# Kernel optimization log

Measured on AMD Instinct MI355X. Metric: run time of the kernel, lower is better.

Reference implementation:

```python
import jax, jax.numpy as jnp
import numpy as np

HIDDEN = 512
HEADS = 8
NORM = 1.0 / np.sqrt(HIDDEN // HEADS)  # torch: 1/sqrt(tensor(dim_k)//head) = 1/8


def setup_inputs() -> dict:
    key = jax.random.key(0)
    ks = jax.random.split(key, 14)
    B, N, D = 2, 2048, HIDDEN
    s = 0.02
    d = {
        "x_re": jax.random.normal(ks[0], (B, N, D), dtype=jnp.float32),
        "x_im": jax.random.normal(ks[1], (B, N, D), dtype=jnp.float32),
    }
    names = ["Wq_re", "Wq_im", "bq_re", "bq_im",
             "Wk_re", "Wk_im", "bk_re", "bk_im",
             "Wv_re", "Wv_im", "bv_re", "bv_im"]
    for i, nm in enumerate(names):
        shape = (D, D) if nm.startswith("W") else (D,)
        d[nm] = jax.random.normal(ks[2 + i], shape, dtype=jnp.float32) * s
    return d


def reference(x_re, x_im,
              Wq_re, Wq_im, bq_re, bq_im,
              Wk_re, Wk_im, bk_re, bk_im,
              Wv_re, Wv_im, bv_re, bv_im):
    B, N, D = x_re.shape
    h, dk = HEADS, D // HEADS
    x = jax.lax.complex(x_re, x_im)
    Wq = jax.lax.complex(Wq_re, Wq_im); bq = jax.lax.complex(bq_re, bq_im)
    Wk = jax.lax.complex(Wk_re, Wk_im); bk = jax.lax.complex(bk_re, bk_im)
    Wv = jax.lax.complex(Wv_re, Wv_im); bv = jax.lax.complex(bv_re, bv_im)

    def proj(W, b):  # torch nn.Linear: x @ W.T + b, then split heads -> [B,h,N,dk]
        y = x @ W.T + b
        return y.reshape(B, N, h, dk).transpose(0, 2, 1, 3)

    q, k, v = proj(Wq, bq), proj(Wk, bk), proj(Wv, bv)
    # complex matmul (no conjugation, matching torch.matmul), scaled
    dist = jnp.einsum("bhnd,bhmd->bhnm", q, k) * NORM
    probs = jax.nn.softmax(jnp.abs(dist), axis=-1).astype(jnp.complex64)
    att = jnp.einsum("bhnm,bhmd->bhnd", probs, v)
    att = att.transpose(0, 2, 1, 3).reshape(B, N, D)
    # real-view output [B, N, D, 2]
    return jnp.stack([att.real, att.imag], axis=-1)
```

## Files before the change

### kernel.cpp

```cpp
#include <hip/hip_runtime.h>
#include <hip/hip_bf16.h>
#include <math.h>

#define B_ 2
#define N_ 2048
#define D_ 512
#define H_ 8
#define DK_ 64
#define M_ (B_ * N_)

typedef short s16x8 __attribute__((ext_vector_type(8)));
typedef short s16x4 __attribute__((ext_vector_type(4)));
typedef float fx4   __attribute__((ext_vector_type(4)));
typedef int   ix4   __attribute__((ext_vector_type(4)));

static __device__ __forceinline__ short f2bf(float f) {
    __hip_bfloat16 h = __float2bfloat16(f);
    return __builtin_bit_cast(short, h);
}
static __device__ __forceinline__ float bf2f(short s) {
    unsigned int u = ((unsigned int)(unsigned short)s) << 16;
    return __builtin_bit_cast(float, u);
}
static __device__ __forceinline__ float fexp2(float x) {
#if __has_builtin(__builtin_amdgcn_exp2f)
    return __builtin_amdgcn_exp2f(x);
#else
    return exp2f(x);
#endif
}
static __device__ __forceinline__ float fsqrt_(float x) {
#if __has_builtin(__builtin_amdgcn_sqrtf)
    return __builtin_amdgcn_sqrtf(x);
#else
    return sqrtf(x);
#endif
}
static __device__ __forceinline__ int pack_tr(float a, float b) {
    unsigned ua = __builtin_bit_cast(unsigned, a);
    unsigned ub = __builtin_bit_cast(unsigned, b);
    return (int)((ua >> 16) | (ub & 0xFFFF0000u));
}

#define MFMA16(a, b, c) __builtin_amdgcn_mfma_f32_16x16x32_bf16(a, b, c, 0, 0, 0)

#define C2_ 0.18033688f
#define M0_ 16.0f

__global__ __launch_bounds__(256, 2)
void qkproj_mfma(const float* __restrict__ xr, const float* __restrict__ xi,
                 const float* __restrict__ W0r, const float* __restrict__ W0i,
                 const float* __restrict__ b0r, const float* __restrict__ b0i,
                 const float* __restrict__ W1r, const float* __restrict__ W1i,
                 const float* __restrict__ b1r, const float* __restrict__ b1i,
                 short* __restrict__ o0r, short* __restrict__ o0i,
                 short* __restrict__ o1r, short* __restrict__ o1i)
{
    __shared__ short sA[2][128][40];
    __shared__ short sB[2][64][40];

    const int tid = threadIdx.x;
    const int w = tid >> 6, l = tid & 63, lg = l >> 4, lc = l & 15;
    const int wr = w >> 1, wc = w & 1;
    const int bn = blockIdx.x, bm = blockIdx.y, z = blockIdx.z;
    const float* Wr = z ? W1r : W0r;
    const float* Wi = z ? W1i : W0i;
    const float* br = z ? b1r : b0r;
    const float* bi = z ? b1i : b0i;
    short* outr = z ? o1r : o0r;
    short* outi = z ? o1i : o0i;

    const int srow = tid >> 3, scol = (tid & 7) * 4;
    int aoff = (bm * 128 + srow) * D_ + scol;
    int boff = (bn * 64 + srow) * D_ + scol;

    float4 rA[8], rB[4];
    auto issue = [&]() {
#pragma unroll
        for (int u = 0; u < 8; ++u) {
            const float* src = (u >= 4) ? xi : xr;
            rA[u] = *(const float4*)&src[aoff + (u & 3) * 32 * D_];
        }
#pragma unroll
        for (int u = 0; u < 4; ++u) {
            const float* src = (u >= 2) ? Wi : Wr;
            rB[u] = *(const float4*)&src[boff + (u & 1) * 32 * D_];
        }
        aoff += 32; boff += 32;
    };

    fx4 Cre[4][2], Cim[4][2];
#pragma unroll
    for (int mf = 0; mf < 4; ++mf)
#pragma unroll
        for (int nf = 0; nf < 2; ++nf)
#pragma unroll
            for (int j = 0; j < 4; ++j) { Cre[mf][nf][j] = 0.f; Cim[mf][nf][j] = 0.f; }

    issue();
    for (int k0 = 0; k0 < D_; k0 += 32) {
        __syncthreads();
#pragma unroll
        for (int u = 0; u < 8; ++u) {
            int comp = u >> 2, row = (u & 3) * 32 + srow;
            float vv[4] = {rA[u].x, rA[u].y, rA[u].z, rA[u].w};
            s16x4 hv;
#pragma unroll
            for (int q = 0; q < 4; ++q) hv[q] = f2bf(vv[q]);
            *(s16x4*)&sA[comp][row][scol] = hv;
        }
#pragma unroll
        for (int u = 0; u < 4; ++u) {
            int comp = u >> 1, row = (u & 1) * 32 + srow;
            float vv[4] = {rB[u].x, rB[u].y, rB[u].z, rB[u].w};
            s16x4 hv;
#pragma unroll
            for (int q = 0; q < 4; ++q) hv[q] = f2bf(vv[q]);
            *(s16x4*)&sB[comp][row][scol] = hv;
        }
        __syncthreads();
        if (k0 + 32 < D_) issue();

        s16x8 a[2][4];
#pragma unroll
        for (int comp = 0; comp < 2; ++comp)
#pragma unroll
            for (int mf = 0; mf < 4; ++mf)
                a[comp][mf] = *(const s16x8*)&sA[comp][wr * 64 + mf * 16 + lc][lg * 8];
        s16x8 bfr[2][2], bin[2];
#pragma unroll
        for (int comp = 0; comp < 2; ++comp)
#pragma unroll
            for (int nf = 0; nf < 2; ++nf)
                bfr[comp][nf] = *(const s16x8*)&sB[comp][wc * 32 + nf * 16 + lc][lg * 8];
#pragma unroll
        for (int nf = 0; nf < 2; ++nf) bin[nf] = bfr[1][nf] ^ (short)0x8000;

        __builtin_amdgcn_s_setprio(1);
#pragma unroll
        for (int mf = 0; mf < 4; ++mf)
#pragma unroll
            for (int nf = 0; nf < 2; ++nf) {
                Cre[mf][nf] = MFMA16(a[0][mf], bfr[0][nf], Cre[mf][nf]);
                Cre[mf][nf] = MFMA16(a[1][mf], bin[nf],    Cre[mf][nf]);
                Cim[mf][nf] = MFMA16(a[0][mf], bfr[1][nf], Cim[mf][nf]);
                Cim[mf][nf] = MFMA16(a[1][mf], bfr[0][nf], Cim[mf][nf]);
            }
        __builtin_amdgcn_s_setprio(0);
    }

    const int bb = (bm * 128) >> 11;
#pragma unroll
    for (int nf = 0; nf < 2; ++nf) {
        const int c = bn * 64 + wc * 32 + nf * 16 + lc;
        const float brv = br[c], biv = bi[c];
        const int h = c >> 6, dd = c & 63;
        const int n00 = (bm * 128 + wr * 64 + lg * 4) & (N_ - 1);
        size_t obase = (((size_t)(bb * H_ + h) * N_) + n00) * DK_ + dd;
#pragma unroll
        for (int mf = 0; mf < 4; ++mf)
#pragma unroll
            for (int j = 0; j < 4; ++j) {
                size_t o = obase + (size_t)(mf * 16 + j) * DK_;
                outr[o] = f2bf(Cre[mf][nf][j] + brv);
                outi[o] = f2bf(Cim[mf][nf][j] + biv);
            }
    }
}

__global__ __launch_bounds__(256, 2)
void vproj_mfma(const float* __restrict__ xr, const float* __restrict__ xi,
                const float* __restrict__ Wr, const float* __restrict__ Wi,
                const float* __restrict__ br, const float* __restrict__ bi,
                short* __restrict__ outr, short* __restrict__ outi)
{
    __shared__ short sA[2][2][64][40];
    __shared__ short sB[2][2][64][40];

    const int tid = threadIdx.x;
    const int w = tid >> 6, l = tid & 63, lg = l >> 4, lc = l & 15;
    const int wr = w >> 1, wc = w & 1;
    const int bn = blockIdx.x, bm = blockIdx.y;

    const int srow = tid >> 3, scol = (tid & 7) * 4;
    int aoff = (bm * 64 + srow) * D_ + scol;
    int boff = (bn * 64 + srow) * D_ + scol;

    float4 rA[4], rB[4];
    auto issue = [&]() {
#pragma unroll
        for (int u = 0; u < 4; ++u) {
            const float* src = (u >= 2) ? xi : xr;
            rA[u] = *(const float4*)&src[aoff + (u & 1) * 32 * D_];
        }
#pragma unroll
        for (int u = 0; u < 4; ++u) {
            const float* src = (u >= 2) ? Wi : Wr;
            rB[u] = *(const float4*)&src[boff + (u & 1) * 32 * D_];
        }
        aoff += 32; boff += 32;
    };

    fx4 Cre[2][2], Cim[2][2];
#pragma unroll
    for (int mf = 0; mf < 2; ++mf)
#pragma unroll
        for (int nf = 0; nf < 2; ++nf)
#pragma unroll
            for (int j = 0; j < 4; ++j) { Cre[mf][nf][j] = 0.f; Cim[mf][nf][j] = 0.f; }

    issue();
    for (int k0 = 0; k0 < D_; k0 += 32) {
        __syncthreads();
#pragma unroll
        for (int u = 0; u < 4; ++u) {
            int comp = u >> 1, row = (u & 1) * 32 + srow;
            float vv[4] = {rA[u].x, rA[u].y, rA[u].z, rA[u].w};
            s16x4 hv, lv;
#pragma unroll
            for (int q = 0; q < 4; ++q) {
                short hh = f2bf(vv[q]);
                hv[q] = hh;
                lv[q] = f2bf(vv[q] - bf2f(hh));
            }
            *(s16x4*)&sA[comp][0][row][scol] = hv;
            *(s16x4*)&sA[comp][1][row][scol] = lv;
        }
#pragma unroll
        for (int u = 0; u < 4; ++u) {
            int comp = u >> 1, row = (u & 1) * 32 + srow;
            float vv[4] = {rB[u].x, rB[u].y, rB[u].z, rB[u].w};
            s16x4 hv, lv;
#pragma unroll
            for (int q = 0; q < 4; ++q) {
                short hh = f2bf(vv[q]);
                hv[q] = hh;
                lv[q] = f2bf(vv[q] - bf2f(hh));
            }
            *(s16x4*)&sB[comp][0][row][scol] = hv;
            *(s16x4*)&sB[comp][1][row][scol] = lv;
        }
        __syncthreads();
        if (k0 + 32 < D_) issue();

        s16x8 a[2][2][2];
#pragma unroll
        for (int comp = 0; comp < 2; ++comp)
#pragma unroll
            for (int s = 0; s < 2; ++s)
#pragma unroll
                for (int mf = 0; mf < 2; ++mf)
                    a[comp][s][mf] = *(const s16x8*)&sA[comp][s][wr * 32 + mf * 16 + lc][lg * 8];
        s16x8 bfr[2][2][2], bin[2][2];
#pragma unroll
        for (int comp = 0; comp < 2; ++comp)
#pragma unroll
            for (int s = 0; s < 2; ++s)
#pragma unroll
                for (int nf = 0; nf < 2; ++nf)
                    bfr[comp][s][nf] = *(const s16x8*)&sB[comp][s][wc * 32 + nf * 16 + lc][lg * 8];
#pragma unroll
        for (int s = 0; s < 2; ++s)
#pragma unroll
            for (int nf = 0; nf < 2; ++nf)
                bin[s][nf] = bfr[1][s][nf] ^ (short)0x8000;

        __builtin_amdgcn_s_setprio(1);
#pragma unroll
        for (int mf = 0; mf < 2; ++mf)
#pragma unroll
            for (int nf = 0; nf < 2; ++nf) {
                fx4 cr = Cre[mf][nf], ci = Cim[mf][nf];
                cr = MFMA16(a[0][0][mf], bfr[0][0][nf], cr);
                cr = MFMA16(a[1][0][mf], bin[0][nf],    cr);
                ci = MFMA16(a[0][0][mf], bfr[1][0][nf], ci);
                ci = MFMA16(a[1][0][mf], bfr[0][0][nf], ci);
                cr = MFMA16(a[0][0][mf], bfr[0][1][nf], cr);
                cr = MFMA16(a[0][1][mf], bfr[0][0][nf], cr);
                cr = MFMA16(a[1][0][mf], bin[1][nf],    cr);
                cr = MFMA16(a[1][1][mf], bin[0][nf],    cr);
                ci = MFMA16(a[0][0][mf], bfr[1][1][nf], ci);
                ci = MFMA16(a[0][1][mf], bfr[1][0][nf], ci);
                ci = MFMA16(a[1][0][mf], bfr[0][1][nf], ci);
                ci = MFMA16(a[1][1][mf], bfr[0][0][nf], ci);
                Cre[mf][nf] = cr; Cim[mf][nf] = ci;
            }
        __builtin_amdgcn_s_setprio(0);
    }

    const int bb = (bm * 64) >> 11;
#pragma unroll
    for (int nf = 0; nf < 2; ++nf) {
        const int c = bn * 64 + wc * 32 + nf * 16 + lc;
        const float brv = br[c], biv = bi[c];
        const int h = c >> 6, dd = c & 63;
#pragma unroll
        for (int mf = 0; mf < 2; ++mf) {
            int m0 = bm * 64 + wr * 32 + mf * 16 + lg * 4;
            int n0 = m0 & (N_ - 1);
            s16x4 pr, pi;
#pragma unroll
            for (int j = 0; j < 4; ++j) {
                pr[j] = f2bf(Cre[mf][nf][j] + brv);
                pi[j] = f2bf(Cim[mf][nf][j] + biv);
            }
            size_t o = (((size_t)(bb * H_ + h) * DK_) + dd) * N_ + n0;
            *(s16x4*)&outr[o] = pr;
            *(s16x4*)&outi[o] = pi;
        }
    }
}

#define NT_ (N_ / 64)

static __device__ __forceinline__ int swz8(int row, int slot) {
    return (slot + (row & 7) + 2 * ((row >> 3) & 3)) & 7;
}

__global__ __launch_bounds__(256, 1)
void attn_mfma(const short* __restrict__ qr, const short* __restrict__ qi,
               const short* __restrict__ kr, const short* __restrict__ ki,
               const short* __restrict__ vtr, const short* __restrict__ vti,
               float* __restrict__ out)
{
    __shared__ short sK [2][2][64][64];
    __shared__ short sVt[2][2][64][64];

    const int tid = threadIdx.x;
    const int w = tid >> 6, l = tid & 63, lg = l >> 4, lc = l & 15;

    const int dlin = blockIdx.y * 16 + blockIdx.x;
    const int xcd = dlin & 7, slot = dlin >> 3;
    const int bh = xcd * 2 + (slot >> 4);
    const int qt = slot & 15;
    const int b = bh >> 3, h = bh & 7;

    s16x8 Qr[2][2], Qi_[2][2], Qin[2][2];
#pragma unroll
    for (int qh = 0; qh < 2; ++qh) {
        size_t base = ((size_t)bh * N_ + (size_t)qt * 128 + w * 32 + qh * 16 + lc) * DK_ + lg * 8;
#pragma unroll
        for (int c = 0; c < 2; ++c) {
            Qr[qh][c]  = *(const s16x8*)&qr[base + c * 32];
            Qi_[qh][c] = *(const s16x8*)&qi[base + c * 32];
            Qin[qh][c] = Qi_[qh][c] ^ (short)0x8000;
        }
    }

    s16x8 onesf;
#pragma unroll
    for (int u = 0; u < 8; ++u) onesf[u] = (short)0x3F80;

    fx4 o_re[2][4], o_im[2][4], o_l[2];
#pragma unroll
    for (int qh = 0; qh < 2; ++qh) {
#pragma unroll
        for (int dt = 0; dt < 4; ++dt)
#pragma unroll
            for (int j = 0; j < 4; ++j) { o_re[qh][dt][j] = 0.f; o_im[qh][dt][j] = 0.f; }
#pragma unroll
        for (int j = 0; j < 4; ++j) o_l[qh][j] = 0.f;
    }

    const int rS = ((lc >> 2) << 3) | (lc & 3);
    const int bqs = lg + (lc & 3) + 2 * (lc >> 2);
    const int bvs = lg + (lc & 7) + 2 * (lc >> 3);

    const int srow = tid >> 3, cs = tid & 7;
    const int sw = swz8(srow, cs) * 8;
    int koff = bh * (N_ * DK_) + srow * DK_ + cs * 8;
    int voff = bh * (DK_ * N_) + srow * N_ + cs * 8;

    s16x8 rgK[4], rgV[4];
    auto issue = [&]() {
        rgK[0] = *(const s16x8*)&kr [koff];
        rgK[1] = *(const s16x8*)&kr [koff + 32 * DK_];
        rgK[2] = *(const s16x8*)&ki [koff];
        rgK[3] = *(const s16x8*)&ki [koff + 32 * DK_];
        rgV[0] = *(const s16x8*)&vtr[voff];
        rgV[1] = *(const s16x8*)&vtr[voff + 32 * N_];
        rgV[2] = *(const s16x8*)&vti[voff];
        rgV[3] = *(const s16x8*)&vti[voff + 32 * N_];
        koff += 64 * DK_; voff += 64;
    };
    auto stage = [&](int bi) {
        *(s16x8*)&sK [bi][0][srow     ][sw] = rgK[0];
        *(s16x8*)&sK [bi][0][srow + 32][sw] = rgK[1];
        *(s16x8*)&sK [bi][1][srow     ][sw] = rgK[2];
        *(s16x8*)&sK [bi][1][srow + 32][sw] = rgK[3];
        *(s16x8*)&sVt[bi][0][srow     ][sw] = rgV[0];
        *(s16x8*)&sVt[bi][0][srow + 32][sw] = rgV[1];
        *(s16x8*)&sVt[bi][1][srow     ][sw] = rgV[2];
        *(s16x8*)&sVt[bi][1][srow + 32][sw] = rgV[3];
    };

    issue();
    stage(0);
    for (int kt = 0; kt < NT_; ++kt) {
        const int bi = kt & 1;
        __syncthreads();
        if (kt + 1 < NT_) issue();

        fx4 are[2][4], aim[2][4];
#pragma unroll
        for (int qh = 0; qh < 2; ++qh)
#pragma unroll
            for (int t = 0; t < 4; ++t)
#pragma unroll
                for (int j = 0; j < 4; ++j) { are[qh][t][j] = 0.f; aim[qh][t][j] = 0.f; }

        __builtin_amdgcn_s_setprio(1);
#pragma unroll
        for (int t = 0; t < 4; ++t) {
            const int row = rS + ((t & 1) << 2) + ((t >> 1) << 5);
#pragma unroll
            for (int c = 0; c < 2; ++c) {
                const int sl = ((bqs + 4 * ((c + t) & 1)) & 7) * 8;
                s16x8 Krf = *(const s16x8*)&sK[bi][0][row][sl];
                s16x8 Kif = *(const s16x8*)&sK[bi][1][row][sl];
#pragma unroll
                for (int qh = 0; qh < 2; ++qh) {
                    are[qh][t] = MFMA16(Krf, Qr[qh][c],  are[qh][t]);
                    are[qh][t] = MFMA16(Kif, Qin[qh][c], are[qh][t]);
                    aim[qh][t] = MFMA16(Kif, Qr[qh][c],  aim[qh][t]);
                    aim[qh][t] = MFMA16(Krf, Qi_[qh][c], aim[qh][t]);
                }
            }
        }
        __builtin_amdgcn_s_setprio(0);

        s16x8 Pf[2][2];
#pragma unroll
        for (int qh = 0; qh < 2; ++qh) {
            ix4 w0, w1;
#pragma unroll
            for (int t = 0; t < 4; ++t) {
                float p[4];
#pragma unroll
                for (int j = 0; j < 4; ++j) {
                    float u2 = fmaf(are[qh][t][j], are[qh][t][j], aim[qh][t][j] * aim[qh][t][j]);
                    p[j] = fexp2(fmaf(C2_, fsqrt_(u2), -M0_));
                }
                int d0 = pack_tr(p[0], p[1]);
                int d1 = pack_tr(p[2], p[3]);
                if (t == 0)      { w0[0] = d0; w0[1] = d1; }
                else if (t == 1) { w0[2] = d0; w0[3] = d1; }
                else if (t == 2) { w1[0] = d0; w1[1] = d1; }
                else             { w1[2] = d0; w1[3] = d1; }
            }
            Pf[qh][0] = __builtin_bit_cast(s16x8, w0);
            Pf[qh][1] = __builtin_bit_cast(s16x8, w1);
        }

        __builtin_amdgcn_s_setprio(1);
#pragma unroll
        for (int qh = 0; qh < 2; ++qh) {
            o_l[qh] = MFMA16(Pf[qh][0], onesf, o_l[qh]);
            o_l[qh] = MFMA16(Pf[qh][1], onesf, o_l[qh]);
        }
#pragma unroll
        for (int dt = 0; dt < 4; ++dt) {
            const int d = dt * 16 + lc;
            const int s0 = ((bvs + 4 * dt) & 7) * 8;
            const int s1 = ((bvs + 4 * dt + 4) & 7) * 8;
            s16x8 Vr0 = *(const s16x8*)&sVt[bi][0][d][s0];
            s16x8 Vi0 = *(const s16x8*)&sVt[bi][1][d][s0];
            s16x8 Vr1 = *(const s16x8*)&sVt[bi][0][d][s1];
            s16x8 Vi1 = *(const s16x8*)&sVt[bi][1][d][s1];
#pragma unroll
            for (int qh = 0; qh < 2; ++qh) {
                o_re[qh][dt] = MFMA16(Pf[qh][0], Vr0, o_re[qh][dt]);
                o_im[qh][dt] = MFMA16(Pf[qh][0], Vi0, o_im[qh][dt]);
                o_re[qh][dt] = MFMA16(Pf[qh][1], Vr1, o_re[qh][dt]);
                o_im[qh][dt] = MFMA16(Pf[qh][1], Vi1, o_im[qh][dt]);
            }
        }
        __builtin_amdgcn_s_setprio(0);

        if (kt + 1 < NT_) stage((kt + 1) & 1);
    }

    float2* po = (float2*)out;
#pragma unroll
    for (int qh = 0; qh < 2; ++qh) {
        float inv[4];
#pragma unroll
        for (int j = 0; j < 4; ++j) inv[j] = 1.f / o_l[qh][j];
#pragma unroll
        for (int dt = 0; dt < 4; ++dt)
#pragma unroll
            for (int j = 0; j < 4; ++j) {
                int n  = qt * 128 + w * 32 + qh * 16 + lg * 4 + j;
                int dg = h * 64 + dt * 16 + lc;
                po[((size_t)b * N_ + n) * D_ + dg] =
                    make_float2(o_re[qh][dt][j] * inv[j], o_im[qh][dt][j] * inv[j]);
            }
    }
}

extern "C" void kernel_launch(void* const* d_in, const int* in_sizes, int n_in,
                              void* d_out, int out_size, void* d_ws, size_t ws_size,
                              hipStream_t stream)
{
    const float* xr = (const float*)d_in[0];
    const float* xi = (const float*)d_in[1];
    const float* Wq_r = (const float*)d_in[2];
    const float* Wq_i = (const float*)d_in[3];
    const float* bq_r = (const float*)d_in[4];
    const float* bq_i = (const float*)d_in[5];
    const float* Wk_r = (const float*)d_in[6];
    const float* Wk_i = (const float*)d_in[7];
    const float* bk_r = (const float*)d_in[8];
    const float* bk_i = (const float*)d_in[9];
    const float* Wv_r = (const float*)d_in[10];
    const float* Wv_i = (const float*)d_in[11];
    const float* bv_r = (const float*)d_in[12];
    const float* bv_i = (const float*)d_in[13];

    short* ws = (short*)d_ws;
    const size_t SZ = (size_t)B_ * H_ * N_ * DK_;
    short* qr_  = ws + 0 * SZ;
    short* qi_  = ws + 1 * SZ;
    short* kr_  = ws + 2 * SZ;
    short* ki_  = ws + 3 * SZ;
    short* vtr_ = ws + 4 * SZ;
    short* vti_ = ws + 5 * SZ;

    dim3 qkgrid(D_ / 64, M_ / 128, 2);
    qkproj_mfma<<<qkgrid, 256, 0, stream>>>(xr, xi,
                                            Wq_r, Wq_i, bq_r, bq_i,
                                            Wk_r, Wk_i, bk_r, bk_i,
                                            qr_, qi_, kr_, ki_);
    dim3 vgrid(D_ / 64, M_ / 64);
    vproj_mfma<<<vgrid, 256, 0, stream>>>(xr, xi, Wv_r, Wv_i, bv_r, bv_i, vtr_, vti_);

    dim3 agrid(16, 16);
    attn_mfma<<<agrid, 256, 0, stream>>>(qr_, qi_, kr_, ki_, vtr_, vti_, (float*)d_out);
}
```

Measured before the change: 136.9 us.

## Split attention KV sequence across two wave groups with LDS reduction

Doubles the attention block to 512 threads. The two wave groups each process alternating 64-key tiles of the same 128-row query tile, staged together in a doubled double-buffered LDS. At the end, the partial numerators and denominators are combined through shared memory before normalising and writing. The aim is more waves in flight per CU for latency hiding with a grid of only 256 blocks. The cost is double the LDS, extra reduction syncs, and register pressure under the 512,2 launch bounds.

```diff
diff --git a/kernel.cpp b/kernel.cpp
--- a/kernel.cpp
+++ b/kernel.cpp
@@ -312,22 +312,24 @@
 }
 
 #define NT_ (N_ / 64)
+#define NR_ (NT_ / 2)
 
 static __device__ __forceinline__ int swz8(int row, int slot) {
     return (slot + (row & 7) + 2 * ((row >> 3) & 3)) & 7;
 }
 
-__global__ __launch_bounds__(256, 1)
+__global__ __launch_bounds__(512, 2)
 void attn_mfma(const short* __restrict__ qr, const short* __restrict__ qi,
                const short* __restrict__ kr, const short* __restrict__ ki,
                const short* __restrict__ vtr, const short* __restrict__ vti,
                float* __restrict__ out)
 {
-    __shared__ short sK [2][2][64][64];
-    __shared__ short sVt[2][2][64][64];
+    __shared__ short sK [2][2][2][64][64];
+    __shared__ short sVt[2][2][2][64][64];
 
     const int tid = threadIdx.x;
     const int w = tid >> 6, l = tid & 63, lg = l >> 4, lc = l & 15;
+    const int kg = w & 1, qw = w >> 1;
 
     const int dlin = blockIdx.y * 16 + blockIdx.x;
     const int xcd = dlin & 7, slot = dlin >> 3;
@@ -338,7 +340,7 @@
     s16x8 Qr[2][2], Qi_[2][2], Qin[2][2];
 #pragma unroll
     for (int qh = 0; qh < 2; ++qh) {
-        size_t base = ((size_t)bh * N_ + (size_t)qt * 128 + w * 32 + qh * 16 + lc) * DK_ + lg * 8;
+        size_t base = ((size_t)bh * N_ + (size_t)qt * 128 + qw * 32 + qh * 16 + lc) * DK_ + lg * 8;
 #pragma unroll
         for (int c = 0; c < 2; ++c) {
             Qr[qh][c]  = *(const s16x8*)&qr[base + c * 32];
@@ -371,35 +373,33 @@
     int koff = bh * (N_ * DK_) + srow * DK_ + cs * 8;
     int voff = bh * (DK_ * N_) + srow * N_ + cs * 8;
 
-    s16x8 rgK[4], rgV[4];
+    s16x8 rgK[2][2], rgV[2][2];
     auto issue = [&]() {
-        rgK[0] = *(const s16x8*)&kr [koff];
-        rgK[1] = *(const s16x8*)&kr [koff + 32 * DK_];
-        rgK[2] = *(const s16x8*)&ki [koff];
-        rgK[3] = *(const s16x8*)&ki [koff + 32 * DK_];
-        rgV[0] = *(const s16x8*)&vtr[voff];
-        rgV[1] = *(const s16x8*)&vtr[voff + 32 * N_];
-        rgV[2] = *(const s16x8*)&vti[voff];
-        rgV[3] = *(const s16x8*)&vti[voff + 32 * N_];
-        koff += 64 * DK_; voff += 64;
+#pragma unroll
+        for (int g = 0; g < 2; ++g) {
+            rgK[g][0] = *(const s16x8*)&kr [koff + g * 64 * DK_];
+            rgK[g][1] = *(const s16x8*)&ki [koff + g * 64 * DK_];
+            rgV[g][0] = *(const s16x8*)&vtr[voff + g * 64];
+            rgV[g][1] = *(const s16x8*)&vti[voff + g * 64];
+        }
+        koff += 128 * DK_; voff += 128;
     };
-    auto stage = [&](int bi) {
-        *(s16x8*)&sK [bi][0][srow     ][sw] = rgK[0];
-        *(s16x8*)&sK [bi][0][srow + 32][sw] = rgK[1];
-        *(s16x8*)&sK [bi][1][srow     ][sw] = rgK[2];
-        *(s16x8*)&sK [bi][1][srow + 32][sw] = rgK[3];
-        *(s16x8*)&sVt[bi][0][srow     ][sw] = rgV[0];
-        *(s16x8*)&sVt[bi][0][srow + 32][sw] = rgV[1];
-        *(s16x8*)&sVt[bi][1][srow     ][sw] = rgV[2];
-        *(s16x8*)&sVt[bi][1][srow + 32][sw] = rgV[3];
+    auto stage = [&](int nb) {
+#pragma unroll
+        for (int g = 0; g < 2; ++g)
+#pragma unroll
+            for (int comp = 0; comp < 2; ++comp) {
+                *(s16x8*)&sK [nb][g][comp][srow][sw] = rgK[g][comp];
+                *(s16x8*)&sVt[nb][g][comp][srow][sw] = rgV[g][comp];
+            }
     };
 
     issue();
     stage(0);
-    for (int kt = 0; kt < NT_; ++kt) {
-        const int bi = kt & 1;
-        __syncthreads();
-        if (kt + 1 < NT_) issue();
+    for (int r = 0; r < NR_; ++r) {
+        const int cb = r & 1;
+        __syncthreads();
+        if (r + 1 < NR_) issue();
 
         fx4 are[2][4], aim[2][4];
 #pragma unroll
@@ -416,8 +416,8 @@
 #pragma unroll
             for (int c = 0; c < 2; ++c) {
                 const int sl = ((bqs + 4 * ((c + t) & 1)) & 7) * 8;
-                s16x8 Krf = *(const s16x8*)&sK[bi][0][row][sl];
-                s16x8 Kif = *(const s16x8*)&sK[bi][1][row][sl];
+                s16x8 Krf = *(const s16x8*)&sK[cb][kg][0][row][sl];
+                s16x8 Kif = *(const s16x8*)&sK[cb][kg][1][row][sl];
 #pragma unroll
                 for (int qh = 0; qh < 2; ++qh) {
                     are[qh][t] = MFMA16(Krf, Qr[qh][c],  are[qh][t]);
@@ -463,10 +463,10 @@
             const int d = dt * 16 + lc;
             const int s0 = ((bvs + 4 * dt) & 7) * 8;
             const int s1 = ((bvs + 4 * dt + 4) & 7) * 8;
-            s16x8 Vr0 = *(const s16x8*)&sVt[bi][0][d][s0];
-            s16x8 Vi0 = *(const s16x8*)&sVt[bi][1][d][s0];
-            s16x8 Vr1 = *(const s16x8*)&sVt[bi][0][d][s1];
-            s16x8 Vi1 = *(const s16x8*)&sVt[bi][1][d][s1];
+            s16x8 Vr0 = *(const s16x8*)&sVt[cb][kg][0][d][s0];
+            s16x8 Vi0 = *(const s16x8*)&sVt[cb][kg][1][d][s0];
+            s16x8 Vr1 = *(const s16x8*)&sVt[cb][kg][0][d][s1];
+            s16x8 Vi1 = *(const s16x8*)&sVt[cb][kg][1][d][s1];
 #pragma unroll
             for (int qh = 0; qh < 2; ++qh) {
                 o_re[qh][dt] = MFMA16(Pf[qh][0], Vr0, o_re[qh][dt]);
@@ -477,24 +477,45 @@
         }
         __builtin_amdgcn_s_setprio(0);
 
-        if (kt + 1 < NT_) stage((kt + 1) & 1);
-    }
-
+        if (r + 1 < NR_) stage(cb ^ 1);
+    }
+
+    float* red = (float*)&sK[0][0][0][0][0];
     float2* po = (float2*)out;
 #pragma unroll
     for (int qh = 0; qh < 2; ++qh) {
-        float inv[4];
-#pragma unroll
-        for (int j = 0; j < 4; ++j) inv[j] = 1.f / o_l[qh][j];
-#pragma unroll
-        for (int dt = 0; dt < 4; ++dt)
-#pragma unroll
-            for (int j = 0; j < 4; ++j) {
-                int n  = qt * 128 + w * 32 + qh * 16 + lg * 4 + j;
-                int dg = h * 64 + dt * 16 + lc;
-                po[((size_t)b * N_ + n) * D_ + dg] =
-                    make_float2(o_re[qh][dt][j] * inv[j], o_im[qh][dt][j] * inv[j]);
-            }
+        __syncthreads();
+        if (kg == 1) {
+            const int base = (qw * 64 + l) * 37;
+#pragma unroll
+            for (int dt = 0; dt < 4; ++dt)
+#pragma unroll
+                for (int j = 0; j < 4; ++j) {
+                    red[base + dt * 8 + j * 2 + 0] = o_re[qh][dt][j];
+                    red[base + dt * 8 + j * 2 + 1] = o_im[qh][dt][j];
+                }
+#pragma unroll
+            for (int j = 0; j < 4; ++j) red[base + 32 + j] = o_l[qh][j];
+        }
+        __syncthreads();
+        if (kg == 0) {
+            const int base = (qw * 64 + l) * 37;
+            float inv[4];
+#pragma unroll
+            for (int j = 0; j < 4; ++j)
+                inv[j] = 1.f / (o_l[qh][j] + red[base + 32 + j]);
+#pragma unroll
+            for (int dt = 0; dt < 4; ++dt)
+#pragma unroll
+                for (int j = 0; j < 4; ++j) {
+                    float re = o_re[qh][dt][j] + red[base + dt * 8 + j * 2 + 0];
+                    float im = o_im[qh][dt][j] + red[base + dt * 8 + j * 2 + 1];
+                    int n  = qt * 128 + qw * 32 + qh * 16 + lg * 4 + j;
+                    int dg = h * 64 + dt * 16 + lc;
+                    po[((size_t)b * N_ + n) * D_ + dg] =
+                        make_float2(re * inv[j], im * inv[j]);
+                }
+        }
     }
 }
 
@@ -535,5 +556,5 @@
     vproj_mfma<<<vgrid, 256, 0, stream>>>(xr, xi, Wv_r, Wv_i, bv_r, bv_i, vtr_, vti_);
 
     dim3 agrid(16, 16);
-    attn_mfma<<<agrid, 256, 0, stream>>>(qr_, qi_, kr_, ki_, vtr_, vti_, (float*)d_out);
-}
+    attn_mfma<<<agrid, 512, 0, stream>>>(qr_, qi_, kr_, ki_, vtr_, vti_, (float*)d_out);
+}
```

Result: faster. 120.7 us (median of 2 runs) (-11.8%).
